# Kernel optimization log

Measured on AMD Instinct MI355X. Metric: run time of the kernel, lower is better.

Reference implementation:

```python
import jax, jax.numpy as jnp
import numpy as np
import math

B, C, H, W = 8, 512, 32, 32
NUM_HEADS = 8          # channels // num_head_channels = 512 // 64
NUM_GROUPS = 32        # GroupNorm32
EPS = 1e-5


def setup_inputs() -> dict:
    key = jax.random.key(0)
    k1, k2, k3, k4, k5 = jax.random.split(key, 5)
    x = jax.random.normal(k1, (B, C, H, W), dtype=jnp.float32)
    # GroupNorm affine params (torch init: ones/zeros)
    norm_scale = jnp.ones((C,), dtype=jnp.float32)
    norm_bias = jnp.zeros((C,), dtype=jnp.float32)
    # 1x1 Conv1d weights: qkv maps C -> 3C, proj maps C -> C
    qkv_w = jax.random.normal(k2, (3 * C, C), dtype=jnp.float32) * 0.02
    qkv_b = jax.random.normal(k3, (3 * C,), dtype=jnp.float32) * 0.02
    # NOTE: original zero-inits proj_out; we use small random weights so the
    # block computes non-trivial math (same op structure, same FLOPs).
    proj_w = jax.random.normal(k4, (C, C), dtype=jnp.float32) * 0.02
    proj_b = jax.random.normal(k5, (C,), dtype=jnp.float32) * 0.02
    return {"x": x, "norm_scale": norm_scale, "norm_bias": norm_bias,
            "qkv_w": qkv_w, "qkv_b": qkv_b, "proj_w": proj_w, "proj_b": proj_b}


def _attention_block(x, norm_scale, norm_bias, qkv_w, qkv_b, proj_w, proj_b):
    b, c, h, w = x.shape
    t = h * w
    xf = x.reshape(b, c, t)
    # GroupNorm32: fp32 compute, 32 groups, biased variance, eps=1e-5
    g = xf.astype(jnp.float32).reshape(b, NUM_GROUPS, c // NUM_GROUPS, t)
    mean = g.mean(axis=(2, 3), keepdims=True)
    var = g.var(axis=(2, 3), keepdims=True)
    gn = ((g - mean) * jax.lax.rsqrt(var + EPS)).reshape(b, c, t)
    gn = (gn * norm_scale[None, :, None] + norm_bias[None, :, None]).astype(xf.dtype)
    # 1x1 conv == channel matmul: [B,C,T] -> [B,3C,T]
    qkv = jnp.einsum('oc,bct->bot', qkv_w, gn) + qkv_b[None, :, None]
    # Legacy head layout: [B, H*3*ch, T] -> [B*H, 3*ch, T]
    ch = c // NUM_HEADS
    qkv = qkv.reshape(b * NUM_HEADS, 3 * ch, t)
    q, k, v = jnp.split(qkv, 3, axis=1)          # each [B*H, ch, T]
    scale = 1.0 / math.sqrt(math.sqrt(ch))
    weight = jnp.einsum('bct,bcs->bts', q * scale, k * scale)  # [B*H, T, T]
    weight = jax.nn.softmax(weight.astype(jnp.float32), axis=-1).astype(qkv.dtype)
    a = jnp.einsum('bts,bcs->bct', weight, v).reshape(b, c, t)
    out = jnp.einsum('oc,bct->bot', proj_w, a) + proj_b[None, :, None]
    return (xf + out).reshape(b, c, h, w)


def reference(x, norm_scale, norm_bias, qkv_w, qkv_b, proj_w, proj_b):
    return _attention_block(x, norm_scale, norm_bias, qkv_w, qkv_b, proj_w, proj_b)
```

## Files before the change

kernel.cpp:

```cpp
#include <hip/hip_runtime.h>
#include <math.h>

#define B_   8
#define C_   512
#define T_   1024
#define G_   32
#define CPG  16
#define NH   8
#define OC3  1536
#define EPS  1e-5f

#define QSCALE 0.18033688011112042f
#define C_OFF  11.541560327111708f

typedef __bf16 bf16;
typedef __bf16 bf16x4 __attribute__((ext_vector_type(4)));
typedef __bf16 bf16x8 __attribute__((ext_vector_type(8)));
typedef float  f32x4  __attribute__((ext_vector_type(4)));
typedef short  s16x4  __attribute__((ext_vector_type(4)));

#define MFMA16(a, b, c) __builtin_amdgcn_mfma_f32_16x16x32_bf16((a), (b), (c), 0, 0, 0)

__device__ __forceinline__ f32x4 mfma_k16(bf16x4 a, bf16x4 b, f32x4 c) {
#if __has_builtin(__builtin_amdgcn_mfma_f32_16x16x16_bf16)
    return __builtin_amdgcn_mfma_f32_16x16x16_bf16(a, b, c, 0, 0, 0);
#else
    return __builtin_amdgcn_mfma_f32_16x16x16bf16_1k(
        __builtin_bit_cast(s16x4, a), __builtin_bit_cast(s16x4, b), c, 0, 0, 0);
#endif
}

__device__ __forceinline__ float fexp2(float x) {
#if defined(__has_builtin)
#if __has_builtin(__builtin_amdgcn_exp2f)
    return __builtin_amdgcn_exp2f(x);
#else
    return __expf(x * 0.6931471805599453f);
#endif
#else
    return __expf(x * 0.6931471805599453f);
#endif
}

__global__ __launch_bounds__(256) void pre_kernel(const float* __restrict__ w1,
                                                  bf16* __restrict__ wb1,
                                                  const float* __restrict__ w2,
                                                  bf16* __restrict__ wb2,
                                                  const float* __restrict__ x,
                                                  const float* __restrict__ scale,
                                                  const float* __restrict__ bias,
                                                  bf16* __restrict__ gnT)
{
    const int blk0 = blockIdx.x;
    const int tid = threadIdx.x;
    if (blk0 < 1024) {
        const float* src = (blk0 < 768) ? w1 : w2;
        bf16* dst        = (blk0 < 768) ? wb1 : wb2;
        int i = (blk0 < 768 ? blk0 : blk0 - 768) * 256 + tid;
        float4 v = ((const float4*)src)[i];
        bf16x4 o;
        o[0] = (bf16)v.x; o[1] = (bf16)v.y; o[2] = (bf16)v.z; o[3] = (bf16)v.w;
        *(bf16x4*)(dst + (size_t)i * 4) = o;
        return;
    }
    const int blk = blk0 - 1024;
    const int b = blk >> 5, g = blk & 31;
    const size_t base = (size_t)blk * (CPG * T_);
    const float4* xin = (const float4*)(x + base);

    float s = 0.f, ss = 0.f;
    float4 vals[16];
#pragma unroll
    for (int i = 0; i < 16; ++i) {
        float4 v = xin[tid + i * 256];
        vals[i] = v;
        s  += v.x + v.y + v.z + v.w;
        ss += v.x * v.x + v.y * v.y + v.z * v.z + v.w * v.w;
    }

    __shared__ float rs[256], rss[256];
    rs[tid] = s; rss[tid] = ss;
    __syncthreads();
    for (int off = 128; off > 0; off >>= 1) {
        if (tid < off) { rs[tid] += rs[tid + off]; rss[tid] += rss[tid + off]; }
        __syncthreads();
    }
    const float invN = 1.f / (float)(CPG * T_);
    const float mean = rs[0] * invN;
    const float var  = rss[0] * invN - mean * mean;
    const float inv  = rsqrtf(var + EPS);

    const int c0 = g * CPG;
    float sc[16], bi[16];
#pragma unroll
    for (int i = 0; i < 16; ++i) {
        float s_ = scale[c0 + i] * inv;
        sc[i] = s_;
        bi[i] = bias[c0 + i] - mean * s_;
    }
    bf16* ob = gnT + (size_t)b * (T_ * C_) + c0;
#pragma unroll
    for (int tt = 0; tt < 4; ++tt) {
        bf16x8 lo, hi;
#pragma unroll
        for (int i = 0; i < 8; ++i) {
            float v0 = (tt == 0) ? vals[i].x : (tt == 1) ? vals[i].y
                     : (tt == 2) ? vals[i].z : vals[i].w;
            float v1 = (tt == 0) ? vals[i + 8].x : (tt == 1) ? vals[i + 8].y
                     : (tt == 2) ? vals[i + 8].z : vals[i + 8].w;
            lo[i] = (bf16)(v0 * sc[i] + bi[i]);
            hi[i] = (bf16)(v1 * sc[i + 8] + bi[i + 8]);
        }
        bf16* p = ob + (size_t)(4 * tid + tt) * C_;
        *(bf16x8*)p       = lo;
        *(bf16x8*)(p + 8) = hi;
    }
}

__global__ __launch_bounds__(256) void qkv_mm(const bf16* __restrict__ gnT,
                                              const bf16* __restrict__ Wb,
                                              const float* __restrict__ bias,
                                              bf16* __restrict__ qkvT)
{
    const int b   = blockIdx.z;
    const int o0  = blockIdx.y * 128;
    const int t0  = blockIdx.x * 128;
    const int tid = threadIdx.x;
    const int lane = tid & 63;
    const int w  = tid >> 6;
    const int wr = w >> 1, wc = w & 1;
    const int lq = lane & 15, lg = lane >> 4;

    __shared__ __align__(16) bf16 Ag[128][72];
    __shared__ __align__(16) bf16 Bg[128][72];

    const bf16* gA = gnT + (size_t)b * (T_ * C_) + (size_t)t0 * C_;
    const bf16* gB = Wb + (size_t)o0 * C_;

    f32x4 acc[4][4];
#pragma unroll
    for (int i = 0; i < 4; ++i)
#pragma unroll
        for (int j = 0; j < 4; ++j) { acc[i][j][0]=0.f; acc[i][j][1]=0.f; acc[i][j][2]=0.f; acc[i][j][3]=0.f; }

    bf16x8 areg[4], breg[4];
#pragma unroll
    for (int it = 0; it < 4; ++it) {
        int chunk = it * 256 + tid, row = chunk >> 3, cp = chunk & 7;
        areg[it] = *(const bf16x8*)(gA + (size_t)row * C_ + cp * 8);
        breg[it] = *(const bf16x8*)(gB + (size_t)row * C_ + cp * 8);
    }

    for (int k0 = 0; k0 < C_; k0 += 64) {
        __syncthreads();
#pragma unroll
        for (int it = 0; it < 4; ++it) {
            int chunk = it * 256 + tid, row = chunk >> 3, cp = chunk & 7;
            *(bf16x8*)&Ag[row][cp * 8] = areg[it];
            *(bf16x8*)&Bg[row][cp * 8] = breg[it];
        }
        __syncthreads();
        if (k0 + 64 < C_) {
#pragma unroll
            for (int it = 0; it < 4; ++it) {
                int chunk = it * 256 + tid, row = chunk >> 3, cp = chunk & 7;
                areg[it] = *(const bf16x8*)(gA + (size_t)row * C_ + k0 + 64 + cp * 8);
                breg[it] = *(const bf16x8*)(gB + (size_t)row * C_ + k0 + 64 + cp * 8);
            }
        }
#pragma unroll
        for (int kb = 0; kb < 2; ++kb) {
            bf16x8 af[4], bfr[4];
#pragma unroll
            for (int i = 0; i < 4; ++i) {
                af[i]  = *(const bf16x8*)&Ag[wr * 64 + i * 16 + lq][kb * 32 + lg * 8];
                bfr[i] = *(const bf16x8*)&Bg[wc * 64 + i * 16 + lq][kb * 32 + lg * 8];
            }
#pragma unroll
            for (int mf = 0; mf < 4; ++mf)
#pragma unroll
                for (int nf = 0; nf < 4; ++nf)
                    acc[mf][nf] = MFMA16(af[mf], bfr[nf], acc[mf][nf]);
        }
    }

#pragma unroll
    for (int nf = 0; nf < 4; ++nf) {
        int chg = o0 + wc * 64 + nf * 16 + lq;
        int seg = chg >> 6;
        int which = seg % 3;
        int chs = chg & 63;
        float bv = bias[chg];
        bf16* outb = qkvT + (size_t)(b * 24 + seg) * (T_ * 64);
        if (which != 2) {
            float osc = (which == 0) ? QSCALE : 1.0f;
#pragma unroll
            for (int mf = 0; mf < 4; ++mf) {
                int tb = t0 + wr * 64 + mf * 16 + lg * 4;
#pragma unroll
                for (int r = 0; r < 4; ++r)
                    outb[(size_t)(tb + r) * 64 + chs] = (bf16)((acc[mf][nf][r] + bv) * osc);
            }
        } else {
#pragma unroll
            for (int mf = 0; mf < 4; ++mf) {
                int tb = t0 + wr * 64 + mf * 16 + lg * 4;
                bf16x4 pb;
#pragma unroll
                for (int r = 0; r < 4; ++r) pb[r] = (bf16)(acc[mf][nf][r] + bv);
                *(bf16x4*)(outb + (size_t)chs * T_ + tb) = pb;
            }
        }
    }
}

__global__ __launch_bounds__(256) void proj_mm(const bf16* __restrict__ aT,
                                               const bf16* __restrict__ PWb,
                                               const float* __restrict__ bias,
                                               const float* __restrict__ x,
                                               float* __restrict__ out)
{
    const int b   = blockIdx.z;
    const int o0  = blockIdx.y * 128;
    const int t0  = blockIdx.x * 64;
    const int tid = threadIdx.x;
    const int lane = tid & 63;
    const int w  = tid >> 6;
    const int wr = w >> 1, wc = w & 1;
    const int lq = lane & 15, lg = lane >> 4;

    __shared__ __align__(16) bf16 Ag[64][72];
    __shared__ __align__(16) bf16 Bg[128][72];

    const bf16* gA = aT + (size_t)b * (T_ * C_) + (size_t)t0 * C_;
    const bf16* gB = PWb + (size_t)o0 * C_;

    f32x4 acc[2][4];
#pragma unroll
    for (int i = 0; i < 2; ++i)
#pragma unroll
        for (int j = 0; j < 4; ++j) { acc[i][j][0]=0.f; acc[i][j][1]=0.f; acc[i][j][2]=0.f; acc[i][j][3]=0.f; }

    bf16x8 areg[2], breg[4];
#pragma unroll
    for (int it = 0; it < 2; ++it) {
        int chunk = it * 256 + tid, row = chunk >> 3, cp = chunk & 7;
        areg[it] = *(const bf16x8*)(gA + (size_t)row * C_ + cp * 8);
    }
#pragma unroll
    for (int it = 0; it < 4; ++it) {
        int chunk = it * 256 + tid, row = chunk >> 3, cp = chunk & 7;
        breg[it] = *(const bf16x8*)(gB + (size_t)row * C_ + cp * 8);
    }

    for (int k0 = 0; k0 < C_; k0 += 64) {
        __syncthreads();
#pragma unroll
        for (int it = 0; it < 2; ++it) {
            int chunk = it * 256 + tid, row = chunk >> 3, cp = chunk & 7;
            *(bf16x8*)&Ag[row][cp * 8] = areg[it];
        }
#pragma unroll
        for (int it = 0; it < 4; ++it) {
            int chunk = it * 256 + tid, row = chunk >> 3, cp = chunk & 7;
            *(bf16x8*)&Bg[row][cp * 8] = breg[it];
        }
        __syncthreads();
        if (k0 + 64 < C_) {
#pragma unroll
            for (int it = 0; it < 2; ++it) {
                int chunk = it * 256 + tid, row = chunk >> 3, cp = chunk & 7;
                areg[it] = *(const bf16x8*)(gA + (size_t)row * C_ + k0 + 64 + cp * 8);
            }
#pragma unroll
            for (int it = 0; it < 4; ++it) {
                int chunk = it * 256 + tid, row = chunk >> 3, cp = chunk & 7;
                breg[it] = *(const bf16x8*)(gB + (size_t)row * C_ + k0 + 64 + cp * 8);
            }
        }
#pragma unroll
        for (int kb = 0; kb < 2; ++kb) {
            bf16x8 af[2], bfr[4];
#pragma unroll
            for (int i = 0; i < 2; ++i)
                af[i]  = *(const bf16x8*)&Ag[wr * 32 + i * 16 + lq][kb * 32 + lg * 8];
#pragma unroll
            for (int j = 0; j < 4; ++j)
                bfr[j] = *(const bf16x8*)&Bg[wc * 64 + j * 16 + lq][kb * 32 + lg * 8];
#pragma unroll
            for (int mf = 0; mf < 2; ++mf)
#pragma unroll
                for (int nf = 0; nf < 4; ++nf)
                    acc[mf][nf] = MFMA16(af[mf], bfr[nf], acc[mf][nf]);
        }
    }

#pragma unroll
    for (int nf = 0; nf < 4; ++nf) {
        int o = o0 + wc * 64 + nf * 16 + lq;
        float bv = bias[o];
#pragma unroll
        for (int mf = 0; mf < 2; ++mf) {
            int tb = t0 + wr * 32 + mf * 16 + lg * 4;
            size_t idx = ((size_t)b * C_ + o) * T_ + tb;
            float4 xr = *(const float4*)(x + idx);
            float4 rv;
            rv.x = acc[mf][nf][0] + bv + xr.x;
            rv.y = acc[mf][nf][1] + bv + xr.y;
            rv.z = acc[mf][nf][2] + bv + xr.z;
            rv.w = acc[mf][nf][3] + bv + xr.w;
            *(float4*)(out + idx) = rv;
        }
    }
}

__global__ __launch_bounds__(512) void attn_kernel(const bf16* __restrict__ qkvT,
                                                   bf16* __restrict__ aT)
{
    const int id = blockIdx.x;
    const int bh = id & 63;
    const int tile = id >> 6;
    const int tid = threadIdx.x;
    const int lane = tid & 63;
    const int w  = tid >> 6;
    const int lq = lane & 15;
    const int lg = lane >> 4;
    const int q0 = tile * 128 + w * 16;

    const bf16* qb = qkvT + (size_t)(bh * 3 + 0) * (T_ * 64);
    const bf16* kb = qkvT + (size_t)(bh * 3 + 1) * (T_ * 64);
    const bf16* vb = qkvT + (size_t)(bh * 3 + 2) * (T_ * 64);

    __shared__ __align__(16) bf16 ks[64][72];
    __shared__ __align__(16) bf16 vs[64][136];

    bf16x8 qf[2];
#pragma unroll
    for (int kh = 0; kh < 2; ++kh)
        qf[kh] = *(const bf16x8*)(qb + (size_t)(q0 + lq) * 64 + kh * 32 + lg * 8);

    f32x4 oacc[4], lacc;
    lacc[0]=0.f; lacc[1]=0.f; lacc[2]=0.f; lacc[3]=0.f;
#pragma unroll
    for (int og = 0; og < 4; ++og) { oacc[og][0]=0.f; oacc[og][1]=0.f; oacc[og][2]=0.f; oacc[og][3]=0.f; }

    bf16x4 vones;
    vones[0] = (bf16)1.0f; vones[1] = (bf16)1.0f; vones[2] = (bf16)1.0f; vones[3] = (bf16)1.0f;

    const int sr = tid >> 3, scp = tid & 7;
    bf16x8 kreg, vreg;
    kreg = *(const bf16x8*)(kb + (size_t)sr * 64 + scp * 8);
    vreg = *(const bf16x8*)(vb + (size_t)sr * T_ + scp * 8);

    for (int i = 0; i < 16; ++i) {
        __syncthreads();
        *(bf16x8*)&ks[sr][scp * 8] = kreg;
        *(bf16x8*)&vs[sr][scp * 8] = vreg;
        __syncthreads();
        if (i < 15) {
            int sn = (i + 1) * 64;
            kreg = *(const bf16x8*)(kb + (size_t)(sn + sr) * 64 + scp * 8);
            vreg = *(const bf16x8*)(vb + (size_t)sr * T_ + sn + scp * 8);
        }

        f32x4 st[4];
        f32x4 cinit; cinit[0] = -C_OFF; cinit[1] = -C_OFF; cinit[2] = -C_OFF; cinit[3] = -C_OFF;
#pragma unroll
        for (int g = 0; g < 4; ++g) {
            bf16x8 kf0 = *(const bf16x8*)&ks[g * 16 + lq][lg * 8];
            bf16x8 kf1 = *(const bf16x8*)&ks[g * 16 + lq][32 + lg * 8];
            st[g] = MFMA16(kf0, qf[0], cinit);
            st[g] = MFMA16(kf1, qf[1], st[g]);
        }
        bf16x4 pa16[4];
#pragma unroll
        for (int g = 0; g < 4; ++g)
#pragma unroll
            for (int r = 0; r < 4; ++r)
                pa16[g][r] = (bf16)fexp2(st[g][r]);
#pragma unroll
        for (int g = 0; g < 4; ++g)
            lacc = mfma_k16(pa16[g], vones, lacc);
#pragma unroll
        for (int og = 0; og < 4; ++og) {
#pragma unroll
            for (int g = 0; g < 4; ++g) {
                bf16x4 vf = *(const bf16x4*)&vs[og * 16 + lq][g * 16 + lg * 4];
                oacc[og] = mfma_k16(pa16[g], vf, oacc[og]);
            }
        }
    }

    const int b = bh >> 3, h = bh & 7;
    float li[4];
#pragma unroll
    for (int r = 0; r < 4; ++r) li[r] = 1.f / lacc[r];
    bf16* ob = aT + ((size_t)b * T_ + q0 + lg * 4) * C_ + h * 64 + lq;
#pragma unroll
    for (int og = 0; og < 4; ++og)
#pragma unroll
        for (int r = 0; r < 4; ++r)
            ob[(size_t)r * C_ + og * 16] = (bf16)(oacc[og][r] * li[r]);
}

extern "C" void kernel_launch(void* const* d_in, const int* in_sizes, int n_in,
                              void* d_out, int out_size, void* d_ws, size_t ws_size,
                              hipStream_t stream)
{
    (void)in_sizes; (void)n_in; (void)out_size; (void)ws_size;
    const float* x      = (const float*)d_in[0];
    const float* nscale = (const float*)d_in[1];
    const float* nbias  = (const float*)d_in[2];
    const float* qkv_w  = (const float*)d_in[3];
    const float* qkv_b  = (const float*)d_in[4];
    const float* proj_w = (const float*)d_in[5];
    const float* proj_b = (const float*)d_in[6];
    float* out = (float*)d_out;

    char* wsb = (char*)d_ws;
    bf16*  gnT  = (bf16*) (wsb);
    bf16*  Wb   = (bf16*) (wsb + (size_t)(8  << 20));
    bf16*  PWb  = Wb + (size_t)OC3 * C_;
    bf16*  qkvT = (bf16*) (wsb + (size_t)(12 << 20));
    bf16*  aT   = (bf16*) (wsb + (size_t)(36 << 20));

    pre_kernel<<<1280, 256, 0, stream>>>(qkv_w, Wb, proj_w, PWb,
                                         x, nscale, nbias, gnT);
    qkv_mm<<<dim3(T_ / 128, OC3 / 128, B_), 256, 0, stream>>>(gnT, Wb, qkv_b, qkvT);
    attn_kernel<<<512, 512, 0, stream>>>(qkvT, aT);
    proj_mm<<<dim3(T_ / 64, C_ / 128, B_), 256, 0, stream>>>(aT, PWb, proj_b, x, out);
}
```

Before: 77.98 us.

## Double-buffer K in LDS and load V fragments directly from global memory

K tiles now go into a two-slot LDS buffer, so each iteration needs one barrier instead of two, and the next tile's store overlaps the current compute. V is no longer staged through shared memory. Each lane reads its 8-byte V fragments straight from global memory, which all eight waves in the block read redundantly. This cuts LDS traffic and barriers but relies on L1/L2 caching to absorb the repeated, poorly coalesced V reads.

```diff
diff --git a/kernel.cpp b/kernel.cpp
--- a/kernel.cpp
+++ b/kernel.cpp
@@ -331,8 +331,7 @@
     const bf16* kb = qkvT + (size_t)(bh * 3 + 1) * (T_ * 64);
     const bf16* vb = qkvT + (size_t)(bh * 3 + 2) * (T_ * 64);
 
-    __shared__ __align__(16) bf16 ks[64][72];
-    __shared__ __align__(16) bf16 vs[64][136];
+    __shared__ __align__(16) bf16 ks[2][64][72];
 
     bf16x8 qf[2];
 #pragma unroll
@@ -348,27 +347,38 @@
     vones[0] = (bf16)1.0f; vones[1] = (bf16)1.0f; vones[2] = (bf16)1.0f; vones[3] = (bf16)1.0f;
 
     const int sr = tid >> 3, scp = tid & 7;
-    bf16x8 kreg, vreg;
+    bf16x8 kreg;
     kreg = *(const bf16x8*)(kb + (size_t)sr * 64 + scp * 8);
-    vreg = *(const bf16x8*)(vb + (size_t)sr * T_ + scp * 8);
+    *(bf16x8*)&ks[0][sr][scp * 8] = kreg;
+    kreg = *(const bf16x8*)(kb + (size_t)(64 + sr) * 64 + scp * 8);
+    __syncthreads();
+
+    const bf16* vrow0 = vb + (size_t)(0 * 16 + lq) * T_ + lg * 4;
+    const bf16* vrow1 = vb + (size_t)(1 * 16 + lq) * T_ + lg * 4;
+    const bf16* vrow2 = vb + (size_t)(2 * 16 + lq) * T_ + lg * 4;
+    const bf16* vrow3 = vb + (size_t)(3 * 16 + lq) * T_ + lg * 4;
 
     for (int i = 0; i < 16; ++i) {
-        __syncthreads();
-        *(bf16x8*)&ks[sr][scp * 8] = kreg;
-        *(bf16x8*)&vs[sr][scp * 8] = vreg;
-        __syncthreads();
-        if (i < 15) {
-            int sn = (i + 1) * 64;
-            kreg = *(const bf16x8*)(kb + (size_t)(sn + sr) * 64 + scp * 8);
-            vreg = *(const bf16x8*)(vb + (size_t)sr * T_ + sn + scp * 8);
+        const int cur = i & 1;
+        if (i < 15) *(bf16x8*)&ks[cur ^ 1][sr][scp * 8] = kreg;
+        if (i < 14) kreg = *(const bf16x8*)(kb + (size_t)((i + 2) * 64 + sr) * 64 + scp * 8);
+
+        bf16x4 vf[4][4];
+        const int kbase = i * 64;
+#pragma unroll
+        for (int g = 0; g < 4; ++g) {
+            vf[0][g] = *(const bf16x4*)(vrow0 + kbase + g * 16);
+            vf[1][g] = *(const bf16x4*)(vrow1 + kbase + g * 16);
+            vf[2][g] = *(const bf16x4*)(vrow2 + kbase + g * 16);
+            vf[3][g] = *(const bf16x4*)(vrow3 + kbase + g * 16);
         }
 
         f32x4 st[4];
         f32x4 cinit; cinit[0] = -C_OFF; cinit[1] = -C_OFF; cinit[2] = -C_OFF; cinit[3] = -C_OFF;
 #pragma unroll
         for (int g = 0; g < 4; ++g) {
-            bf16x8 kf0 = *(const bf16x8*)&ks[g * 16 + lq][lg * 8];
-            bf16x8 kf1 = *(const bf16x8*)&ks[g * 16 + lq][32 + lg * 8];
+            bf16x8 kf0 = *(const bf16x8*)&ks[cur][g * 16 + lq][lg * 8];
+            bf16x8 kf1 = *(const bf16x8*)&ks[cur][g * 16 + lq][32 + lg * 8];
             st[g] = MFMA16(kf0, qf[0], cinit);
             st[g] = MFMA16(kf1, qf[1], st[g]);
         }
@@ -382,13 +392,12 @@
         for (int g = 0; g < 4; ++g)
             lacc = mfma_k16(pa16[g], vones, lacc);
 #pragma unroll
-        for (int og = 0; og < 4; ++og) {
-#pragma unroll
-            for (int g = 0; g < 4; ++g) {
-                bf16x4 vf = *(const bf16x4*)&vs[og * 16 + lq][g * 16 + lg * 4];
-                oacc[og] = mfma_k16(pa16[g], vf, oacc[og]);
-            }
-        }
+        for (int og = 0; og < 4; ++og)
+#pragma unroll
+            for (int g = 0; g < 4; ++g)
+                oacc[og] = mfma_k16(pa16[g], vf[og][g], oacc[og]);
+
+        __syncthreads();
     }
 
     const int b = bh >> 3, h = bh & 7;
```

Result: slower. 165.9 us (+112.8%).
